# Performance work log

Measured on AMD Instinct MI355X. Metric: run time of the kernel, lower is better.

The kernel has to match this reference:

```python
import jax, jax.numpy as jnp
import numpy as np
from jax import lax

DN = ('NCHW', 'OIHW', 'NCHW')

def _conv(x, w, b, stride):
    y = lax.conv_general_dilated(x, w, (stride, stride), [(1, 1), (1, 1)], dimension_numbers=DN)
    return y + b[None, :, None, None]

def _deconv(x, w, b):
    # ConvTranspose2d(k=4, stride=2, pad=1) == conv with lhs_dilation=2, pad=k-1-p=2,
    # with w already in flipped OIHW layout.
    y = lax.conv_general_dilated(x, w, (1, 1), [(2, 2), (2, 2)], lhs_dilation=(2, 2), dimension_numbers=DN)
    return y + b[None, :, None, None]

def setup_inputs() -> dict:
    key = jax.random.key(0)
    ks = jax.random.split(key, 14)
    s = 0.05  # keep activations numerically tame
    return {
        'x':   jax.random.normal(ks[0], (16, 3, 256, 256), jnp.float32),
        'ew1': jax.random.normal(ks[1], (64, 3, 4, 4), jnp.float32) * s,
        'eb1': jax.random.normal(ks[2], (64,), jnp.float32) * s,
        'ew2': jax.random.normal(ks[3], (128, 64, 4, 4), jnp.float32) * s,
        'eb2': jax.random.normal(ks[4], (128,), jnp.float32) * s,
        'ew3': jax.random.normal(ks[5], (256, 128, 4, 4), jnp.float32) * s,
        'eb3': jax.random.normal(ks[6], (256,), jnp.float32) * s,
        'cb':  jax.random.normal(ks[7], (8192, 256), jnp.float32),
        'dw1': jax.random.normal(ks[8], (128, 256, 4, 4), jnp.float32) * s,
        'db1': jax.random.normal(ks[9], (128,), jnp.float32) * s,
        'dw2': jax.random.normal(ks[10], (64, 128, 4, 4), jnp.float32) * s,
        'db2': jax.random.normal(ks[11], (64,), jnp.float32) * s,
        'dw3': jax.random.normal(ks[12], (3, 64, 4, 4), jnp.float32) * s,
        'db3': jax.random.normal(ks[13], (3,), jnp.float32) * s,
    }

def reference(x, ew1, eb1, ew2, eb2, ew3, eb3, cb, dw1, db1, dw2, db2, dw3, db3):
    # encoder: 3 stride-2 convs with ReLU between
    h = jax.nn.relu(_conv(x, ew1, eb1, 2))
    h = jax.nn.relu(_conv(h, ew2, eb2, 2))
    feat = _conv(h, ew3, eb3, 2)                     # [B, 256, 32, 32]
    B, C, H, W = feat.shape
    flat = feat.reshape(B, C, H * W).transpose(0, 2, 1)  # [B, HW, C]
    scores = jnp.einsum('btc,kc->btk', flat, cb)     # [B, HW, K] large matrix
    indices = jnp.argmax(scores, axis=-1)            # [B, HW]
    quantized = cb[indices]                          # [B, HW, C]
    q = quantized.transpose(0, 2, 1).reshape(B, C, H, W)
    # decoder: 3 stride-2 transposed convs with ReLU between
    d = jax.nn.relu(_deconv(q, dw1, db1))
    d = jax.nn.relu(_deconv(d, dw2, db2))
    recon = _deconv(d, dw3, db3)                     # [B, 3, 256, 256]
    return recon, indices
```

## Files before the change

kernel.cpp:

```cpp
#include <hip/hip_runtime.h>
#include <hip/hip_fp16.h>
#include <cstdint>
#include <cstddef>

typedef __attribute__((ext_vector_type(8))) short short8;
typedef __attribute__((ext_vector_type(8))) _Float16 h16x8;
typedef __attribute__((ext_vector_type(4))) float f32x4;

__device__ __forceinline__ short f2bf(float x) {
  union { float f; unsigned u; } a; a.f = x;
  unsigned r = a.u + 0x7fff + ((a.u >> 16) & 1);
  return (short)(r >> 16);
}
__device__ __forceinline__ float bf2f(short s) {
  union { unsigned u; float f; } a;
  a.u = ((unsigned)(unsigned short)s) << 16; return a.f;
}
__device__ __forceinline__ void fsplit16(float v, short& h, short& l) {
  __half a = __float2half(v);
  h = (short)__half_as_ushort(a);
  l = (short)__half_as_ushort(__float2half(v - __half2float(a)));
}

__device__ __forceinline__ void ld16(const void* g, void* l) {
  __builtin_amdgcn_global_load_lds(
      (const __attribute__((address_space(1))) unsigned int*)g,
      (__attribute__((address_space(3))) unsigned int*)l, 16, 0, 0);
}

__global__ __launch_bounds__(256) void conv1_kernel(
    const float* __restrict__ x, const float* __restrict__ w,
    const float* __restrict__ bias, short* __restrict__ yh, short* __restrict__ yl)
{
  __shared__ __align__(16) float wl[64 * 48];
  __shared__ float bl[64];
  const int tid = threadIdx.x;
  for (int i = tid; i < 64 * 48; i += 256) wl[i] = w[i];
  if (tid < 64) bl[tid] = bias[tid];
  __syncthreads();
  const int n  = blockIdx.y;
  const int oh = blockIdx.x * 2 + (tid >> 7);
  const int ow = tid & 127;
  const float* xb = x + (size_t)n * 3 * 65536;
  const int ih0 = oh * 2 - 1, iw0 = ow * 2 - 1;
  float xin[48];
#pragma unroll
  for (int ic = 0; ic < 3; ++ic)
#pragma unroll
    for (int kh = 0; kh < 4; ++kh) {
      int ih = ih0 + kh;
      bool rok = (unsigned)ih < 256u;
#pragma unroll
      for (int kw = 0; kw < 4; ++kw) {
        int iw = iw0 + kw;
        xin[ic * 16 + kh * 4 + kw] =
            (rok && (unsigned)iw < 256u) ? xb[ic * 65536 + ih * 256 + iw] : 0.f;
      }
    }
  const size_t ob = ((size_t)n * 16384 + oh * 128 + ow) * 64;
  for (int g = 0; g < 8; ++g) {
    short hs[8], ls[8];
#pragma unroll
    for (int j = 0; j < 8; ++j) {
      const int oc = g * 8 + j;
      float acc = bl[oc];
      const float* wo = &wl[oc * 48];
#pragma unroll
      for (int t = 0; t < 48; ++t) acc = fmaf(wo[t], xin[t], acc);
      acc = fmaxf(acc, 0.f) * 64.f;
      fsplit16(acc, hs[j], ls[j]);
    }
    *(short8*)(yh + ob + g * 8) = *(short8*)hs;
    *(short8*)(yl + ob + g * 8) = *(short8*)ls;
  }
}

template <int COUT, int CIN>
__global__ __launch_bounds__(256) void wpack_conv(
    const float* __restrict__ w, short* __restrict__ Wh, short* __restrict__ Wl)
{
  constexpr int K = 16 * CIN;
  const int idx = blockIdx.x * 256 + threadIdx.x;
  const int oc = idx / K, k = idx - oc * K;
  const int kk = k / CIN, ic = k - kk * CIN;
  const int kh = kk >> 2, kw = kk & 3;
  float v = w[(((size_t)oc * CIN + ic) * 4 + kh) * 4 + kw] * 64.f;
  short h, l;
  fsplit16(v, h, l);
  Wh[idx] = h;
  Wl[idx] = l;
}

template <int CIN, int HIN, int COUTT, bool RELU, bool OUTF>
__global__ __launch_bounds__(256) void conv_mfma(
    const short* __restrict__ inh, const short* __restrict__ inl,
    const short* __restrict__ Wph, const short* __restrict__ Wpl,
    const float* __restrict__ bias,
    short* __restrict__ outh, short* __restrict__ outl,
    float* __restrict__ outf)
{
  constexpr int K = 16 * CIN;
  constexpr int HOUT = HIN / 2;
  constexpr int MT = 128, NPX = 128;
  constexpr int GS = (HOUT == 64) ? 6 : 5;
  constexpr int AE = 4 * MT;
  constexpr int NS = K / 32;
  constexpr float RS = 1.f / 4096.f;
  __shared__ __align__(16) short AhL[2][AE * 8];
  __shared__ __align__(16) short AlL[2][AE * 8];
  __shared__ __align__(16) float bl[MT];
  const int tid = threadIdx.x;
  const int w = tid >> 6, lane = tid & 63;
  const int wm = w >> 1, wn = w & 1;
  const int kgl = lane >> 4, cl = lane & 15;
  const int n = blockIdx.z;
  const int oc0 = blockIdx.y * MT;
  const int oh0 = blockIdx.x * (NPX / HOUT);
  if (tid < MT) bl[tid] = bias[oc0 + tid];

  f32x4 acc[4][4];
#pragma unroll
  for (int i = 0; i < 4; ++i)
#pragma unroll
    for (int j = 0; j < 4; ++j) acc[i][j] = (f32x4){0.f, 0.f, 0.f, 0.f};

  auto stageA = [&](int s, int b) {
    const int kc = s * 32;
#pragma unroll
    for (int rep = 0; rep < AE / 256; ++rep) {
      int e = rep * 256 + tid;
      int kg = e >> 7, oc_l = e & (MT - 1);
      size_t go = (size_t)(oc0 + oc_l) * K + kc + kg * 8;
      int lo = (e & ~63) * 8;
      ld16(Wph + go, &AhL[b][lo]);
      ld16(Wpl + go, &AlL[b][lo]);
    }
  };
  const h16x8 zzh = {0, 0, 0, 0, 0, 0, 0, 0};
  auto loadB = [&](int s, h16x8* bh, h16x8* blv) {
    const int kc = s * 32;
    const int kk = kc / CIN, ic0 = kc % CIN;
    const int kh = kk >> 2, kw = kk & 3;
#pragma unroll
    for (int nt = 0; nt < 4; ++nt) {
      int m = wn * 64 + nt * 16 + cl;
      int ih = 2 * (oh0 + (m >> GS)) - 1 + kh;
      int iw = 2 * (m & (HOUT - 1)) - 1 + kw;
      bool ok = ((unsigned)ih < (unsigned)HIN) && ((unsigned)iw < (unsigned)HIN);
      size_t go = ok ? ((size_t)((n * HIN + ih) * HIN + iw) * CIN + ic0 + kgl * 8)
                     : (size_t)(ic0 + kgl * 8);
      h16x8 vh = *(const h16x8*)(inh + go);
      h16x8 vl = *(const h16x8*)(inl + go);
      bh[nt] = ok ? vh : zzh;
      blv[nt] = ok ? vl : zzh;
    }
  };
  auto compute = [&](int b, const h16x8* bh, const h16x8* blv) {
    h16x8 ah[4], al[4];
#pragma unroll
    for (int mt = 0; mt < 4; ++mt) {
      int row = kgl * MT + wm * 64 + mt * 16 + cl;
      ah[mt] = *(const h16x8*)&AhL[b][row * 8];
      al[mt] = *(const h16x8*)&AlL[b][row * 8];
    }
#pragma unroll
    for (int mt = 0; mt < 4; ++mt)
#pragma unroll
      for (int nt = 0; nt < 4; ++nt) {
        acc[mt][nt] = __builtin_amdgcn_mfma_f32_16x16x32_f16(
            ah[mt], bh[nt], acc[mt][nt], 0, 0, 0);
        acc[mt][nt] = __builtin_amdgcn_mfma_f32_16x16x32_f16(
            ah[mt], blv[nt], acc[mt][nt], 0, 0, 0);
        acc[mt][nt] = __builtin_amdgcn_mfma_f32_16x16x32_f16(
            al[mt], bh[nt], acc[mt][nt], 0, 0, 0);
      }
  };

  h16x8 bhA[4], blA[4], bhB[4], blB[4];
  stageA(0, 0);
  loadB(0, bhA, blA);
  __syncthreads();
  for (int s2 = 0; s2 < NS; s2 += 2) {
    stageA(s2 + 1, 1);
    loadB(s2 + 1, bhB, blB);
    compute(0, bhA, blA);
    __syncthreads();
    if (s2 + 2 < NS) { stageA(s2 + 2, 0); loadB(s2 + 2, bhA, blA); }
    compute(1, bhB, blB);
    __syncthreads();
  }
#pragma unroll
  for (int mt = 0; mt < 4; ++mt) {
    const int oc = wm * 64 + mt * 16 + kgl * 4;
    const float4 bv = *(const float4*)&bl[oc];
#pragma unroll
    for (int nt = 0; nt < 4; ++nt) {
      const int px = wn * 64 + nt * 16 + cl;
      const int oh = oh0 + (px >> GS), ow = px & (HOUT - 1);
      const size_t ob =
          ((size_t)n * (HOUT * HOUT) + oh * HOUT + ow) * COUTT + oc0 + oc;
      float v0 = acc[mt][nt][0] * RS + bv.x;
      float v1 = acc[mt][nt][1] * RS + bv.y;
      float v2 = acc[mt][nt][2] * RS + bv.z;
      float v3 = acc[mt][nt][3] * RS + bv.w;
      if (RELU) {
        v0 = fmaxf(v0, 0.f); v1 = fmaxf(v1, 0.f);
        v2 = fmaxf(v2, 0.f); v3 = fmaxf(v3, 0.f);
      }
      if constexpr (OUTF) {
        ushort4 s;
        s.x = __half_as_ushort(__float2half(v0));
        s.y = __half_as_ushort(__float2half(v1));
        s.z = __half_as_ushort(__float2half(v2));
        s.w = __half_as_ushort(__float2half(v3));
        *(ushort4*)((unsigned short*)outh + ob) = s;
        *(float4*)(outf + ob) = make_float4(v0, v1, v2, v3);
      } else {
        short4 hh, ll;
        fsplit16(v0 * 64.f, hh.x, ll.x);
        fsplit16(v1 * 64.f, hh.y, ll.y);
        fsplit16(v2 * 64.f, hh.z, ll.z);
        fsplit16(v3 * 64.f, hh.w, ll.w);
        *(short4*)(outh + ob) = hh;
        *(short4*)(outl + ob) = ll;
      }
    }
  }
}

__global__ __launch_bounds__(256) void cb_convert(
    const float* __restrict__ cb, short* __restrict__ cbh,
    short* __restrict__ cbl, short* __restrict__ cb16)
{
  const int g = blockIdx.x * 256 + threadIdx.x;
  const float* p = cb + (size_t)g * 8;
  short hs[8], ls[8], fs[8];
#pragma unroll
  for (int u = 0; u < 8; ++u) {
    float v = p[u];
    short h = f2bf(v);
    hs[u] = h;
    ls[u] = f2bf(v - bf2f(h));
    fs[u] = (short)__half_as_ushort(__float2half(v));
  }
  *(short8*)(cbh + (size_t)g * 8) = *(short8*)hs;
  *(short8*)(cbl + (size_t)g * 8) = *(short8*)ls;
  *(short8*)(cb16 + (size_t)g * 8) = *(short8*)fs;
}

__global__ __launch_bounds__(256, 2) void vq_mfma(
    const short* __restrict__ cb16, const short* __restrict__ ft16,
    float4* __restrict__ t4v)
{
  __shared__ __align__(16) short Ah[3][4 * 128 * 8];
  __shared__ __align__(16) float MrgV[256 * 4];
  const int tid = threadIdx.x;
  const int w = tid >> 6, lane = tid & 63;
  const int wm = w >> 1, wn = w & 1;
  const int tok0 = blockIdx.x * 128;
  const int split = blockIdx.y;
  const int kgl = lane >> 4, cl = lane & 15;
  const int i0 = w * 128;

  h16x8 breg[8][4];
#pragma unroll
  for (int s = 0; s < 8; ++s)
#pragma unroll
    for (int nt = 0; nt < 4; ++nt)
      breg[s][nt] = *(const h16x8*)(ft16 +
          ((size_t)(tok0 + wn * 64 + nt * 16 + cl)) * 256 + s * 32 + kgl * 8);

  auto stageA = [&](int g, int b) {
    const int tile = g >> 3, s = g & 7;
    const int code0 = split * 1024 + tile * 128;
    const int kc = s * 32;
#pragma unroll
    for (int rep = 0; rep < 2; ++rep) {
      int ib = i0 + rep * 64;
      int i = ib + lane;
      int m = i & 127, kg = i >> 7;
      size_t go = (size_t)(code0 + m) * 256 + kc + kg * 8;
      ld16(cb16 + go, &Ah[b][ib * 8]);
    }
  };

  f32x4 acc[4][4];

  float m1[4], m2[4];
#pragma unroll
  for (int nt = 0; nt < 4; ++nt) { m1[nt] = -3.4e38f; m2[nt] = -3.4e38f; }
  const unsigned orbase0 = (unsigned)(wm * 64 + kgl * 4);
  auto fold = [&](int tile) {
    const unsigned orb = (unsigned)(tile * 128) + orbase0;
#pragma unroll
    for (int nt = 0; nt < 4; ++nt)
#pragma unroll
      for (int mt = 0; mt < 4; ++mt)
#pragma unroll
        for (int r = 0; r < 4; ++r) {
          union { float f; unsigned u; } pv;
          pv.f = acc[mt][nt][r];
          pv.u = (pv.u & 0xFFFFF800u) | (orb + (unsigned)(mt * 16 + r));
          float t = fminf(m1[nt], pv.f);
          m1[nt] = fmaxf(m1[nt], pv.f);
          m2[nt] = fmaxf(m2[nt], t);
        }
  };

  auto computeS = [&](int b, int s_static, bool first) {
    h16x8 ah[4];
#pragma unroll
    for (int mt = 0; mt < 4; ++mt) {
      int row = wm * 64 + mt * 16 + cl;
      ah[mt] = *(const h16x8*)&Ah[b][(kgl * 128 + row) * 8];
    }
    if (first) {
      f32x4 z4 = (f32x4){0.f, 0.f, 0.f, 0.f};
#pragma unroll
      for (int mt = 0; mt < 4; ++mt)
#pragma unroll
        for (int nt = 0; nt < 4; ++nt)
          acc[mt][nt] = __builtin_amdgcn_mfma_f32_16x16x32_f16(
              ah[mt], breg[s_static][nt], z4, 0, 0, 0);
    } else {
#pragma unroll
      for (int mt = 0; mt < 4; ++mt)
#pragma unroll
        for (int nt = 0; nt < 4; ++nt)
          acc[mt][nt] = __builtin_amdgcn_mfma_f32_16x16x32_f16(
              ah[mt], breg[s_static][nt], acc[mt][nt], 0, 0, 0);
    }
  };

  stageA(0, 0);
  stageA(1, 1);
  asm volatile("s_waitcnt vmcnt(0)" ::: "memory");
  __builtin_amdgcn_sched_barrier(0);
  __builtin_amdgcn_s_barrier();
  for (int tile = 0; tile < 7; ++tile) {
#pragma unroll
    for (int s = 0; s < 8; ++s) {
      const int g = tile * 8 + s;
      asm volatile("s_waitcnt vmcnt(2)" ::: "memory");
      __builtin_amdgcn_sched_barrier(0);
      __builtin_amdgcn_s_barrier();
      computeS(g % 3, s, s == 0);
      stageA(g + 2, (g + 2) % 3);
    }
    fold(tile);
  }
#pragma unroll
  for (int s = 0; s < 8; ++s) {
    const int g = 56 + s;
    if (s < 7) {
      asm volatile("s_waitcnt vmcnt(2)" ::: "memory");
    } else {
      asm volatile("s_waitcnt vmcnt(0)" ::: "memory");
    }
    __builtin_amdgcn_sched_barrier(0);
    __builtin_amdgcn_s_barrier();
    computeS(g % 3, s, s == 0);
    if (g + 2 < 64) stageA(g + 2, (g + 2) % 3);
  }
  fold(7);

#pragma unroll
  for (int nt = 0; nt < 4; ++nt) {
    float mv[4] = {m1[nt], m2[nt], -3.4e38f, -3.4e38f};
#pragma unroll
    for (int st = 16; st < 64; st <<= 1) {
      float ov[4];
#pragma unroll
      for (int k = 0; k < 4; ++k) ov[k] = __shfl_xor(mv[k], st);
#pragma unroll
      for (int k = 0; k < 4; ++k) {
        if (ov[k] > mv[3]) {
          mv[3] = ov[k];
#pragma unroll
          for (int q = 3; q > 0; --q)
            if (mv[q] > mv[q - 1]) {
              float tv = mv[q]; mv[q] = mv[q - 1]; mv[q - 1] = tv;
            }
        }
      }
    }
    if (lane < 16) {
      int tl = wn * 64 + nt * 16 + cl;
#pragma unroll
      for (int k = 0; k < 4; ++k) MrgV[(wm * 128 + tl) * 4 + k] = mv[k];
    }
  }
  __syncthreads();
  if (tid < 128) {
    int tl = tid;
    float mv[4];
#pragma unroll
    for (int k = 0; k < 4; ++k) mv[k] = MrgV[tl * 4 + k];
#pragma unroll
    for (int k = 0; k < 4; ++k) {
      float ov = MrgV[(128 + tl) * 4 + k];
      if (ov > mv[3]) {
        mv[3] = ov;
#pragma unroll
        for (int q = 3; q > 0; --q)
          if (mv[q] > mv[q - 1]) {
            float tv = mv[q]; mv[q] = mv[q - 1]; mv[q - 1] = tv;
          }
      }
    }
    size_t o = (size_t)split * 16384 + tok0 + tl;
    t4v[o] = make_float4(mv[0], mv[1], mv[2], mv[3]);
  }
}

__global__ __launch_bounds__(256) void vq_rescore(
    const float4* __restrict__ t4v, const float* __restrict__ featc,
    const float* __restrict__ cb, int* __restrict__ fidx,
    float* __restrict__ idx_out)
{
  const int t = blockIdx.x * 256 + threadIdx.x;
  float vs[4] = {-3.4e38f, -3.4e38f, -3.4e38f, -3.4e38f};
  int is[4] = {0, 0, 0, 0};
#pragma unroll
  for (int sp = 0; sp < 8; ++sp) {
    float4 v4 = t4v[(size_t)sp * 16384 + t];
    float vv[4] = {v4.x, v4.y, v4.z, v4.w};
#pragma unroll
    for (int k = 0; k < 4; ++k) {
      float v = vv[k];
      union { float f; unsigned u; } pu; pu.f = v;
      int ii = sp * 1024 + (int)(pu.u & 0x7FFu);
      if (v > vs[3]) {
        vs[3] = v; is[3] = ii;
#pragma unroll
        for (int q = 3; q > 0; --q)
          if (vs[q] > vs[q - 1]) {
            float tv = vs[q]; vs[q] = vs[q - 1]; vs[q - 1] = tv;
            int ti = is[q]; is[q] = is[q - 1]; is[q - 1] = ti;
          }
      }
    }
  }
  const float4* fc = (const float4*)(featc + (size_t)t * 256);
  const float4* c0 = (const float4*)(cb + (size_t)is[0] * 256);
  const float4* c1 = (const float4*)(cb + (size_t)is[1] * 256);
  const float4* c2 = (const float4*)(cb + (size_t)is[2] * 256);
  const float4* c3 = (const float4*)(cb + (size_t)is[3] * 256);
  float s0 = 0.f, s1 = 0.f, s2 = 0.f, s3 = 0.f;
  for (int k4 = 0; k4 < 64; ++k4) {
    float4 f = fc[k4];
    float4 w0 = c0[k4], w1 = c1[k4], w2 = c2[k4], w3 = c3[k4];
    s0 = fmaf(w0.x, f.x, fmaf(w0.y, f.y, fmaf(w0.z, f.z, fmaf(w0.w, f.w, s0))));
    s1 = fmaf(w1.x, f.x, fmaf(w1.y, f.y, fmaf(w1.z, f.z, fmaf(w1.w, f.w, s1))));
    s2 = fmaf(w2.x, f.x, fmaf(w2.y, f.y, fmaf(w2.z, f.z, fmaf(w2.w, f.w, s2))));
    s3 = fmaf(w3.x, f.x, fmaf(w3.y, f.y, fmaf(w3.z, f.z, fmaf(w3.w, f.w, s3))));
  }
  float best = s0; int bi = is[0];
  float sv[3] = {s1, s2, s3};
  int si2[3] = {is[1], is[2], is[3]};
#pragma unroll
  for (int c = 0; c < 3; ++c)
    if (sv[c] > best || (sv[c] == best && si2[c] < bi)) { best = sv[c]; bi = si2[c]; }
  fidx[t] = bi;
  idx_out[t] = (float)bi;
}

template <int COUT, int CIN>
__global__ __launch_bounds__(256) void wpack(
    const float* __restrict__ w, short* __restrict__ Ah, short* __restrict__ Al)
{
  constexpr int K = 4 * CIN;
  const int idx = blockIdx.x * 256 + threadIdx.x;
  const int par = idx / (COUT * K);
  const int rem = idx % (COUT * K);
  const int oc = rem / K;
  const int k = rem % K;
  const int kk = k / CIN, ic = k % CIN;
  const int kh = 2 * (kk >> 1) + (par >> 1);
  const int kw = 2 * (kk & 1) + (par & 1);
  float v = w[(((size_t)oc * CIN + ic) * 4 + kh) * 4 + kw];
  short h = f2bf(v);
  Ah[idx] = h;
  Al[idx] = f2bf(v - bf2f(h));
}

__global__ __launch_bounds__(256) void gather2(
    const short* __restrict__ cbh, const short* __restrict__ cbl,
    const int* __restrict__ fidx, short* __restrict__ qTh, short* __restrict__ qTl)
{
  const int tid = threadIdx.x;
  const int gt = blockIdx.x * 64 + (tid >> 2);
  const int part = tid & 3;
  const int code = fidx[gt];
  const short8* sh = (const short8*)(cbh + (size_t)code * 256 + part * 64);
  const short8* sl = (const short8*)(cbl + (size_t)code * 256 + part * 64);
  short8* dh = (short8*)(qTh + (size_t)gt * 256 + part * 64);
  short8* dl = (short8*)(qTl + (size_t)gt * 256 + part * 64);
#pragma unroll
  for (int j = 0; j < 8; ++j) { dh[j] = sh[j]; dl[j] = sl[j]; }
}

template <int CIN, int GRID, int COUT, int NPX, int WM, int WN, bool OUT_HALF>
__global__ __launch_bounds__(256) void deconv_mfma(
    const short* __restrict__ inh, const short* __restrict__ inl,
    const short* __restrict__ Aph, const short* __restrict__ Apl,
    const float* __restrict__ bias, void* __restrict__ out_h,
    void* __restrict__ out_l)
{
  constexpr int K = 4 * CIN, HOUT = 2 * GRID, AE = 4 * COUT;
  constexpr int GS = (GRID == 32) ? 5 : 6;
  constexpr int NS = K / 32;
  __shared__ __align__(16) short AhL[2][AE * 8];
  __shared__ __align__(16) short AlL[2][AE * 8];
  __shared__ float bl[COUT];
  const int tid = threadIdx.x;
  const int w = tid >> 6, lane = tid & 63;
  const int wm = w / WN, wn = w % WN;
  const int kgl = lane >> 4, cl = lane & 15;
  const int par = blockIdx.y, n = blockIdx.z;
  const int pr = par >> 1, pc = par & 1;
  const int Ut0 = blockIdx.x * (NPX / GRID);
  if (tid < COUT) bl[tid] = bias[tid];

  f32x4 acc[4][4];
#pragma unroll
  for (int i = 0; i < 4; ++i)
#pragma unroll
    for (int j = 0; j < 4; ++j) acc[i][j] = (f32x4){0.f, 0.f, 0.f, 0.f};

  auto stageA = [&](int s, int b) {
    const int kc = s * 32;
#pragma unroll
    for (int rep = 0; rep < AE / 256; ++rep) {
      int e = rep * 256 + tid;
      int kg = e / COUT, oc_l = e % COUT;
      size_t go = ((size_t)(par * COUT + oc_l)) * K + kc + kg * 8;
      int lo = (e & ~63) * 8;
      ld16(Aph + go, &AhL[b][lo]);
      ld16(Apl + go, &AlL[b][lo]);
    }
  };
  const short8 zz = {0, 0, 0, 0, 0, 0, 0, 0};
  auto loadB = [&](int s, short8* bh, short8* blo) {
    const int kc = s * 32;
    const int kk = kc / CIN, ic0 = kc % CIN;
    const int dr = (kk >> 1) + pr - 1, dc = (kk & 1) + pc - 1;
#pragma unroll
    for (int nt = 0; nt < 4; ++nt) {
      int m = wn * 64 + nt * 16 + cl;
      int sU = Ut0 + (m >> GS) + dr;
      int sV = (m & (GRID - 1)) + dc;
      bool ok = (unsigned)sU < (unsigned)GRID && (unsigned)sV < (unsigned)GRID;
      long pix = (long)(n * GRID + sU) * GRID + sV;
      size_t go = ok ? (size_t)(pix * CIN + ic0 + kgl * 8)
                     : (size_t)(ic0 + kgl * 8);
      short8 vh = *(const short8*)(inh + go);
      short8 vl = *(const short8*)(inl + go);
      bh[nt] = ok ? vh : zz;
      blo[nt] = ok ? vl : zz;
    }
  };
  auto compute = [&](int b, const short8* bh, const short8* blo) {
    short8 ah[4], al[4];
#pragma unroll
    for (int mt = 0; mt < 4; ++mt) {
      int row = kgl * COUT + wm * 64 + mt * 16 + cl;
      ah[mt] = *(const short8*)&AhL[b][row * 8];
      al[mt] = *(const short8*)&AlL[b][row * 8];
    }
#pragma unroll
    for (int mt = 0; mt < 4; ++mt)
#pragma unroll
      for (int nt = 0; nt < 4; ++nt) {
        acc[mt][nt] = __builtin_amdgcn_mfma_f32_16x16x32_bf16(
            ah[mt], bh[nt], acc[mt][nt], 0, 0, 0);
        acc[mt][nt] = __builtin_amdgcn_mfma_f32_16x16x32_bf16(
            ah[mt], blo[nt], acc[mt][nt], 0, 0, 0);
        acc[mt][nt] = __builtin_amdgcn_mfma_f32_16x16x32_bf16(
            al[mt], bh[nt], acc[mt][nt], 0, 0, 0);
      }
  };

  short8 bhA[4], blA[4], bhB[4], blB[4];
  stageA(0, 0);
  loadB(0, bhA, blA);
  __syncthreads();
  for (int s2 = 0; s2 < NS; s2 += 2) {
    stageA(s2 + 1, 1);
    loadB(s2 + 1, bhB, blB);
    compute(0, bhA, blA);
    __syncthreads();
    if (s2 + 2 < NS) { stageA(s2 + 2, 0); loadB(s2 + 2, bhA, blA); }
    compute(1, bhB, blB);
    __syncthreads();
  }
#pragma unroll
  for (int mt = 0; mt < 4; ++mt) {
    const int oc = wm * 64 + mt * 16 + kgl * 4;
    const float4 bv = *(const float4*)&bl[oc];
#pragma unroll
    for (int nt = 0; nt < 4; ++nt) {
      const int px = wn * 64 + nt * 16 + cl;
      const int U = Ut0 + (px >> GS), V = px & (GRID - 1);
      const int r = 2 * U + pr, c = 2 * V + pc;
      const size_t ob = ((size_t)n * HOUT * HOUT + (size_t)r * HOUT + c) * COUT + oc;
      float v0 = fmaxf(acc[mt][nt][0] + bv.x, 0.f);
      float v1 = fmaxf(acc[mt][nt][1] + bv.y, 0.f);
      float v2 = fmaxf(acc[mt][nt][2] + bv.z, 0.f);
      float v3 = fmaxf(acc[mt][nt][3] + bv.w, 0.f);
      if constexpr (OUT_HALF) {
        ushort4 s;
        s.x = __half_as_ushort(__float2half(v0));
        s.y = __half_as_ushort(__float2half(v1));
        s.z = __half_as_ushort(__float2half(v2));
        s.w = __half_as_ushort(__float2half(v3));
        *(ushort4*)((unsigned short*)out_h + ob) = s;
      } else {
        short4 hh, ll;
        hh.x = f2bf(v0); ll.x = f2bf(v0 - bf2f(hh.x));
        hh.y = f2bf(v1); ll.y = f2bf(v1 - bf2f(hh.y));
        hh.z = f2bf(v2); ll.z = f2bf(v2 - bf2f(hh.z));
        hh.w = f2bf(v3); ll.w = f2bf(v3 - bf2f(hh.w));
        *(short4*)((short*)out_h + ob) = hh;
        *(short4*)((short*)out_l + ob) = ll;
      }
    }
  }
}

__global__ __launch_bounds__(256) void deconv3_kernel(
    const __half* __restrict__ d2, const float* __restrict__ w,
    const float* __restrict__ bias, float* __restrict__ y)
{
  __shared__ __align__(16) float Xl[108 * 68];
  __shared__ __align__(16) float wl[4 * 4 * 3 * 64];
  const int tid = threadIdx.x;
  for (int i = tid; i < 3072; i += 256) {
    int oc = i >> 10, ic = (i >> 4) & 63, kh = (i >> 2) & 3, kw = i & 3;
    int par = (kh & 1) * 2 + (kw & 1), kidx = (kh >> 1) * 2 + (kw >> 1);
    wl[((par * 4 + kidx) * 3 + oc) * 64 + ic] = w[i];
  }
  const int n = blockIdx.z, r0 = blockIdx.y * 8, c0 = blockIdx.x * 32;
  const int gr0 = (r0 >> 1) - 1, gc0 = (c0 >> 1) - 1;
  for (int e = tid; e < 1728; e += 256) {
    int pl = e >> 4, sub = e & 15;
    int rr = pl / 18, cc = pl - rr * 18;
    int gr = gr0 + rr, gc = gc0 + cc;
    float4 v = make_float4(0.f, 0.f, 0.f, 0.f);
    if ((unsigned)gr < 128u && (unsigned)gc < 128u) {
      const __half2* p =
          (const __half2*)(d2 + ((size_t)(n * 16384 + gr * 128 + gc) * 64 + sub * 4));
      float2 f0 = __half22float2(p[0]);
      float2 f1 = __half22float2(p[1]);
      v = make_float4(f0.x, f0.y, f1.x, f1.y);
    }
    *(float4*)&Xl[pl * 68 + sub * 4] = v;
  }
  __syncthreads();
  const int wv = tid >> 6, lane = tid & 63;
  const int pr = wv >> 1, pc = wv & 1;
  const int Ul = lane >> 4, Vl = lane & 15;
  float a0 = bias[0], a1 = bias[1], a2 = bias[2];
  const int parb = wv * 768;
#pragma unroll
  for (int ic4 = 0; ic4 < 16; ++ic4) {
    float4 xv[4];
#pragma unroll
    for (int t = 0; t < 4; ++t) {
      int lr = Ul + (t >> 1) + pr, lc = Vl + (t & 1) + pc;
      xv[t] = *(const float4*)&Xl[(lr * 18 + lc) * 68 + ic4 * 4];
    }
#pragma unroll
    for (int t = 0; t < 4; ++t) {
      float4 w0 = *(const float4*)&wl[parb + (t * 3 + 0) * 64 + ic4 * 4];
      float4 w1 = *(const float4*)&wl[parb + (t * 3 + 1) * 64 + ic4 * 4];
      float4 w2 = *(const float4*)&wl[parb + (t * 3 + 2) * 64 + ic4 * 4];
      a0 = fmaf(w0.x, xv[t].x, fmaf(w0.y, xv[t].y, fmaf(w0.z, xv[t].z, fmaf(w0.w, xv[t].w, a0))));
      a1 = fmaf(w1.x, xv[t].x, fmaf(w1.y, xv[t].y, fmaf(w1.z, xv[t].z, fmaf(w1.w, xv[t].w, a1))));
      a2 = fmaf(w2.x, xv[t].x, fmaf(w2.y, xv[t].y, fmaf(w2.z, xv[t].z, fmaf(w2.w, xv[t].w, a2))));
    }
  }
  const int r = r0 + 2 * Ul + pr, c = c0 + 2 * Vl + pc;
  float* yn = y + (size_t)n * 3 * 65536 + r * 256 + c;
  yn[0] = a0;
  yn[65536] = a1;
  yn[131072] = a2;
}

extern "C" void kernel_launch(void* const* d_in, const int* in_sizes, int n_in,
                              void* d_out, int out_size, void* d_ws, size_t ws_size,
                              hipStream_t stream)
{
  const float* x   = (const float*)d_in[0];
  const float* ew1 = (const float*)d_in[1];
  const float* eb1 = (const float*)d_in[2];
  const float* ew2 = (const float*)d_in[3];
  const float* eb2 = (const float*)d_in[4];
  const float* ew3 = (const float*)d_in[5];
  const float* eb3 = (const float*)d_in[6];
  const float* cb  = (const float*)d_in[7];
  const float* dw1 = (const float*)d_in[8];
  const float* db1 = (const float*)d_in[9];
  const float* dw2 = (const float*)d_in[10];
  const float* db2 = (const float*)d_in[11];
  const float* dw3 = (const float*)d_in[12];
  const float* db3 = (const float*)d_in[13];

  float* recon = (float*)d_out;
  float* idxf  = (float*)d_out + 3145728;

  const size_t MB = 1048576ull;
  char* ws = (char*)d_ws;
  short* h1h = (short*)ws;
  short* h1l = (short*)(ws + 32 * MB);
  short* h2h = (short*)(ws + 64 * MB);
  short* h2l = (short*)(ws + 80 * MB);
  short* ft16  = (short*)ws;
  float* featf = (float*)(ws + 16 * MB);
  short* cbh  = (short*)(ws + 64 * MB);
  short* cbl  = (short*)(ws + 68 * MB);
  short* cb16 = (short*)(ws + 72 * MB);
  float4* t4v = (float4*)(ws + 80 * MB);
  int*    fidx = (int*)(ws + 92 * MB);
  short* A1h = (short*)(ws + 76 * MB);
  short* A1l = (short*)(ws + 77 * MB);
  short* A2h = (short*)(ws + 78 * MB);
  short* A2l = (short*)(ws + 78 * MB + 262144);
  short* qTh = (short*)ws;
  short* qTl = (short*)(ws + 8 * MB);
  short* d1h = (short*)(ws + 32 * MB);
  short* d1l = (short*)(ws + 48 * MB);
  __half* d2 = (__half*)ws;
  short* W2h = (short*)recon;
  short* W2l = W2h + 131072;
  short* W3h = W2h + 262144;
  short* W3l = W2h + 786432;

  conv1_kernel<<<dim3(64, 16), 256, 0, stream>>>(x, ew1, eb1, h1h, h1l);
  wpack_conv<128, 64><<<dim3(512), 256, 0, stream>>>(ew2, W2h, W2l);
  conv_mfma<64, 128, 128, true, false><<<dim3(32, 1, 16), 256, 0, stream>>>(
      h1h, h1l, W2h, W2l, eb2, h2h, h2l, nullptr);
  wpack_conv<256, 128><<<dim3(2048), 256, 0, stream>>>(ew3, W3h, W3l);
  conv_mfma<128, 64, 256, false, true><<<dim3(8, 2, 16), 256, 0, stream>>>(
      h2h, h2l, W3h, W3l, eb3, ft16, nullptr, featf);

  cb_convert<<<dim3(1024), 256, 0, stream>>>(cb, cbh, cbl, cb16);
  vq_mfma<<<dim3(128, 8), 256, 0, stream>>>(cb16, ft16, t4v);
  vq_rescore<<<dim3(64), 256, 0, stream>>>(t4v, featf, cb, fidx, idxf);

  wpack<128, 256><<<dim3(2048), 256, 0, stream>>>(dw1, A1h, A1l);
  wpack<64, 128><<<dim3(512), 256, 0, stream>>>(dw2, A2h, A2l);
  gather2<<<dim3(256), 256, 0, stream>>>(cbh, cbl, fidx, qTh, qTl);

  deconv_mfma<256, 32, 128, 128, 2, 2, false>
      <<<dim3(8, 4, 16), 256, 0, stream>>>(qTh, qTl, A1h, A1l, db1, d1h, d1l);
  deconv_mfma<128, 64, 64, 256, 1, 4, true>
      <<<dim3(16, 4, 16), 256, 0, stream>>>(d1h, d1l, A2h, A2l, db2, d2, d2);
  deconv3_kernel<<<dim3(8, 32, 16), 256, 0, stream>>>(d2, dw3, db3, recon);
}
```

Before: 828.0 us.

## Triple-buffer LDS stages with explicit vmcnt waits and single barrier per step

The conv and deconv MFMA kernels move from double-buffered LDS staging with two __syncthreads per pair of k-steps to a triple-buffered ring. Each step now uses an explicit s_waitcnt vmcnt on the outstanding async global-to-LDS loads plus one s_barrier. Loads for step s+2 are issued right after computing step s, so two stages stay in flight and the memory latency is better hidden. In exchange, LDS use per block grows by half, which may lower occupancy. The hand-coded vmcnt counts must match the exact number of loads each stage issues, or the kernels can read stale data.

```diff
diff --git a/kernel.cpp b/kernel.cpp
--- a/kernel.cpp
+++ b/kernel.cpp
@@ -106,8 +106,8 @@
   constexpr int AE = 4 * MT;
   constexpr int NS = K / 32;
   constexpr float RS = 1.f / 4096.f;
-  __shared__ __align__(16) short AhL[2][AE * 8];
-  __shared__ __align__(16) short AlL[2][AE * 8];
+  __shared__ __align__(16) short AhL[3][AE * 8];
+  __shared__ __align__(16) short AlL[3][AE * 8];
   __shared__ __align__(16) float bl[MT];
   const int tid = threadIdx.x;
   const int w = tid >> 6, lane = tid & 63;
@@ -179,15 +179,23 @@
   h16x8 bhA[4], blA[4], bhB[4], blB[4];
   stageA(0, 0);
   loadB(0, bhA, blA);
-  __syncthreads();
+  stageA(1, 1);
+  loadB(1, bhB, blB);
   for (int s2 = 0; s2 < NS; s2 += 2) {
-    stageA(s2 + 1, 1);
-    loadB(s2 + 1, bhB, blB);
-    compute(0, bhA, blA);
-    __syncthreads();
-    if (s2 + 2 < NS) { stageA(s2 + 2, 0); loadB(s2 + 2, bhA, blA); }
-    compute(1, bhB, blB);
-    __syncthreads();
+    asm volatile("s_waitcnt vmcnt(12)" ::: "memory");
+    __builtin_amdgcn_sched_barrier(0);
+    __builtin_amdgcn_s_barrier();
+    compute(s2 % 3, bhA, blA);
+    if (s2 + 2 < NS) { stageA(s2 + 2, (s2 + 2) % 3); loadB(s2 + 2, bhA, blA); }
+    if (s2 + 2 < NS) {
+      asm volatile("s_waitcnt vmcnt(12)" ::: "memory");
+    } else {
+      asm volatile("s_waitcnt vmcnt(0)" ::: "memory");
+    }
+    __builtin_amdgcn_sched_barrier(0);
+    __builtin_amdgcn_s_barrier();
+    compute((s2 + 1) % 3, bhB, blB);
+    if (s2 + 3 < NS) { stageA(s2 + 3, (s2 + 3) % 3); loadB(s2 + 3, bhB, blB); }
   }
 #pragma unroll
   for (int mt = 0; mt < 4; ++mt) {
@@ -510,8 +518,9 @@
   constexpr int K = 4 * CIN, HOUT = 2 * GRID, AE = 4 * COUT;
   constexpr int GS = (GRID == 32) ? 5 : 6;
   constexpr int NS = K / 32;
-  __shared__ __align__(16) short AhL[2][AE * 8];
-  __shared__ __align__(16) short AlL[2][AE * 8];
+  constexpr int VC = (AE / 256) * 2 + 8;
+  __shared__ __align__(16) short AhL[3][AE * 8];
+  __shared__ __align__(16) short AlL[3][AE * 8];
   __shared__ float bl[COUT];
   const int tid = threadIdx.x;
   const int w = tid >> 6, lane = tid & 63;
@@ -584,15 +593,31 @@
   short8 bhA[4], blA[4], bhB[4], blB[4];
   stageA(0, 0);
   loadB(0, bhA, blA);
-  __syncthreads();
+  stageA(1, 1);
+  loadB(1, bhB, blB);
   for (int s2 = 0; s2 < NS; s2 += 2) {
-    stageA(s2 + 1, 1);
-    loadB(s2 + 1, bhB, blB);
-    compute(0, bhA, blA);
-    __syncthreads();
-    if (s2 + 2 < NS) { stageA(s2 + 2, 0); loadB(s2 + 2, bhA, blA); }
-    compute(1, bhB, blB);
-    __syncthreads();
+    if constexpr (VC == 12) {
+      asm volatile("s_waitcnt vmcnt(12)" ::: "memory");
+    } else {
+      asm volatile("s_waitcnt vmcnt(10)" ::: "memory");
+    }
+    __builtin_amdgcn_sched_barrier(0);
+    __builtin_amdgcn_s_barrier();
+    compute(s2 % 3, bhA, blA);
+    if (s2 + 2 < NS) { stageA(s2 + 2, (s2 + 2) % 3); loadB(s2 + 2, bhA, blA); }
+    if (s2 + 2 < NS) {
+      if constexpr (VC == 12) {
+        asm volatile("s_waitcnt vmcnt(12)" ::: "memory");
+      } else {
+        asm volatile("s_waitcnt vmcnt(10)" ::: "memory");
+      }
+    } else {
+      asm volatile("s_waitcnt vmcnt(0)" ::: "memory");
+    }
+    __builtin_amdgcn_sched_barrier(0);
+    __builtin_amdgcn_s_barrier();
+    compute((s2 + 1) % 3, bhB, blB);
+    if (s2 + 3 < NS) { stageA(s2 + 3, (s2 + 3) % 3); loadB(s2 + 3, bhB, blB); }
   }
 #pragma unroll
   for (int mt = 0; mt < 4; ++mt) {
```

New measurement: 860.8 us. +4.0%, slower.

## Load conv/deconv weight fragments directly from global, dropping LDS staging and barriers

Applied to the files above, without the earlier changes.

Both the encoder conv and decoder deconv MFMA kernels stop staging weight tiles into double-buffered shared memory. Each lane now reads its A fragments straight from global memory through precomputed row pointers inside a simple K loop unrolled by two. Bias is also read from global in the epilogue. This removes the LDS traffic and __syncthreads barriers and frees LDS for occupancy. In exchange, warps sharing the same weights issue redundant global loads, and the explicit software prefetch of the next stage is gone, so latency hiding now depends on the compiler and on occupancy.

```diff
diff --git a/kernel.cpp b/kernel.cpp
--- a/kernel.cpp
+++ b/kernel.cpp
@@ -103,12 +103,8 @@
   constexpr int HOUT = HIN / 2;
   constexpr int MT = 128, NPX = 128;
   constexpr int GS = (HOUT == 64) ? 6 : 5;
-  constexpr int AE = 4 * MT;
   constexpr int NS = K / 32;
   constexpr float RS = 1.f / 4096.f;
-  __shared__ __align__(16) short AhL[2][AE * 8];
-  __shared__ __align__(16) short AlL[2][AE * 8];
-  __shared__ __align__(16) float bl[MT];
   const int tid = threadIdx.x;
   const int w = tid >> 6, lane = tid & 63;
   const int wm = w >> 1, wn = w & 1;
@@ -116,7 +112,6 @@
   const int n = blockIdx.z;
   const int oc0 = blockIdx.y * MT;
   const int oh0 = blockIdx.x * (NPX / HOUT);
-  if (tid < MT) bl[tid] = bias[oc0 + tid];
 
   f32x4 acc[4][4];
 #pragma unroll
@@ -124,26 +119,33 @@
 #pragma unroll
     for (int j = 0; j < 4; ++j) acc[i][j] = (f32x4){0.f, 0.f, 0.f, 0.f};
 
-  auto stageA = [&](int s, int b) {
-    const int kc = s * 32;
-#pragma unroll
-    for (int rep = 0; rep < AE / 256; ++rep) {
-      int e = rep * 256 + tid;
-      int kg = e >> 7, oc_l = e & (MT - 1);
-      size_t go = (size_t)(oc0 + oc_l) * K + kc + kg * 8;
-      int lo = (e & ~63) * 8;
-      ld16(Wph + go, &AhL[b][lo]);
-      ld16(Wpl + go, &AlL[b][lo]);
-    }
-  };
+  const short* pWh[4];
+  const short* pWl[4];
+#pragma unroll
+  for (int mt = 0; mt < 4; ++mt) {
+    size_t ro = (size_t)(oc0 + wm * 64 + mt * 16 + cl) * K + kgl * 8;
+    pWh[mt] = Wph + ro;
+    pWl[mt] = Wpl + ro;
+  }
   const h16x8 zzh = {0, 0, 0, 0, 0, 0, 0, 0};
-  auto loadB = [&](int s, h16x8* bh, h16x8* blv) {
+  int bm[4];
+#pragma unroll
+  for (int nt = 0; nt < 4; ++nt) bm[nt] = wn * 64 + nt * 16 + cl;
+
+#pragma unroll 2
+  for (int s = 0; s < NS; ++s) {
     const int kc = s * 32;
     const int kk = kc / CIN, ic0 = kc % CIN;
     const int kh = kk >> 2, kw = kk & 3;
+    h16x8 ah[4], al[4], bh[4], blv[4];
+#pragma unroll
+    for (int mt = 0; mt < 4; ++mt) {
+      ah[mt] = *(const h16x8*)(pWh[mt] + kc);
+      al[mt] = *(const h16x8*)(pWl[mt] + kc);
+    }
 #pragma unroll
     for (int nt = 0; nt < 4; ++nt) {
-      int m = wn * 64 + nt * 16 + cl;
+      int m = bm[nt];
       int ih = 2 * (oh0 + (m >> GS)) - 1 + kh;
       int iw = 2 * (m & (HOUT - 1)) - 1 + kw;
       bool ok = ((unsigned)ih < (unsigned)HIN) && ((unsigned)iw < (unsigned)HIN);
@@ -154,15 +156,6 @@
       bh[nt] = ok ? vh : zzh;
       blv[nt] = ok ? vl : zzh;
     }
-  };
-  auto compute = [&](int b, const h16x8* bh, const h16x8* blv) {
-    h16x8 ah[4], al[4];
-#pragma unroll
-    for (int mt = 0; mt < 4; ++mt) {
-      int row = kgl * MT + wm * 64 + mt * 16 + cl;
-      ah[mt] = *(const h16x8*)&AhL[b][row * 8];
-      al[mt] = *(const h16x8*)&AlL[b][row * 8];
-    }
 #pragma unroll
     for (int mt = 0; mt < 4; ++mt)
 #pragma unroll
@@ -174,25 +167,11 @@
         acc[mt][nt] = __builtin_amdgcn_mfma_f32_16x16x32_f16(
             al[mt], bh[nt], acc[mt][nt], 0, 0, 0);
       }
-  };
-
-  h16x8 bhA[4], blA[4], bhB[4], blB[4];
-  stageA(0, 0);
-  loadB(0, bhA, blA);
-  __syncthreads();
-  for (int s2 = 0; s2 < NS; s2 += 2) {
-    stageA(s2 + 1, 1);
-    loadB(s2 + 1, bhB, blB);
-    compute(0, bhA, blA);
-    __syncthreads();
-    if (s2 + 2 < NS) { stageA(s2 + 2, 0); loadB(s2 + 2, bhA, blA); }
-    compute(1, bhB, blB);
-    __syncthreads();
   }
 #pragma unroll
   for (int mt = 0; mt < 4; ++mt) {
     const int oc = wm * 64 + mt * 16 + kgl * 4;
-    const float4 bv = *(const float4*)&bl[oc];
+    const float4 bv = *(const float4*)&bias[oc0 + oc];
 #pragma unroll
     for (int nt = 0; nt < 4; ++nt) {
       const int px = wn * 64 + nt * 16 + cl;
@@ -507,12 +486,9 @@
     const float* __restrict__ bias, void* __restrict__ out_h,
     void* __restrict__ out_l)
 {
-  constexpr int K = 4 * CIN, HOUT = 2 * GRID, AE = 4 * COUT;
+  constexpr int K = 4 * CIN, HOUT = 2 * GRID;
   constexpr int GS = (GRID == 32) ? 5 : 6;
   constexpr int NS = K / 32;
-  __shared__ __align__(16) short AhL[2][AE * 8];
-  __shared__ __align__(16) short AlL[2][AE * 8];
-  __shared__ float bl[COUT];
   const int tid = threadIdx.x;
   const int w = tid >> 6, lane = tid & 63;
   const int wm = w / WN, wn = w % WN;
@@ -520,7 +496,6 @@
   const int par = blockIdx.y, n = blockIdx.z;
   const int pr = par >> 1, pc = par & 1;
   const int Ut0 = blockIdx.x * (NPX / GRID);
-  if (tid < COUT) bl[tid] = bias[tid];
 
   f32x4 acc[4][4];
 #pragma unroll
@@ -528,26 +503,33 @@
 #pragma unroll
     for (int j = 0; j < 4; ++j) acc[i][j] = (f32x4){0.f, 0.f, 0.f, 0.f};
 
-  auto stageA = [&](int s, int b) {
-    const int kc = s * 32;
-#pragma unroll
-    for (int rep = 0; rep < AE / 256; ++rep) {
-      int e = rep * 256 + tid;
-      int kg = e / COUT, oc_l = e % COUT;
-      size_t go = ((size_t)(par * COUT + oc_l)) * K + kc + kg * 8;
-      int lo = (e & ~63) * 8;
-      ld16(Aph + go, &AhL[b][lo]);
-      ld16(Apl + go, &AlL[b][lo]);
-    }
-  };
+  const short* pAh[4];
+  const short* pAl[4];
+#pragma unroll
+  for (int mt = 0; mt < 4; ++mt) {
+    size_t ro = ((size_t)(par * COUT + wm * 64 + mt * 16 + cl)) * K + kgl * 8;
+    pAh[mt] = Aph + ro;
+    pAl[mt] = Apl + ro;
+  }
   const short8 zz = {0, 0, 0, 0, 0, 0, 0, 0};
-  auto loadB = [&](int s, short8* bh, short8* blo) {
+  int bm[4];
+#pragma unroll
+  for (int nt = 0; nt < 4; ++nt) bm[nt] = wn * 64 + nt * 16 + cl;
+
+#pragma unroll 2
+  for (int s = 0; s < NS; ++s) {
     const int kc = s * 32;
     const int kk = kc / CIN, ic0 = kc % CIN;
     const int dr = (kk >> 1) + pr - 1, dc = (kk & 1) + pc - 1;
+    short8 ah[4], al[4], bh[4], blo[4];
+#pragma unroll
+    for (int mt = 0; mt < 4; ++mt) {
+      ah[mt] = *(const short8*)(pAh[mt] + kc);
+      al[mt] = *(const short8*)(pAl[mt] + kc);
+    }
 #pragma unroll
     for (int nt = 0; nt < 4; ++nt) {
-      int m = wn * 64 + nt * 16 + cl;
+      int m = bm[nt];
       int sU = Ut0 + (m >> GS) + dr;
       int sV = (m & (GRID - 1)) + dc;
       bool ok = (unsigned)sU < (unsigned)GRID && (unsigned)sV < (unsigned)GRID;
@@ -559,15 +541,6 @@
       bh[nt] = ok ? vh : zz;
       blo[nt] = ok ? vl : zz;
     }
-  };
-  auto compute = [&](int b, const short8* bh, const short8* blo) {
-    short8 ah[4], al[4];
-#pragma unroll
-    for (int mt = 0; mt < 4; ++mt) {
-      int row = kgl * COUT + wm * 64 + mt * 16 + cl;
-      ah[mt] = *(const short8*)&AhL[b][row * 8];
-      al[mt] = *(const short8*)&AlL[b][row * 8];
-    }
 #pragma unroll
     for (int mt = 0; mt < 4; ++mt)
 #pragma unroll
@@ -579,25 +552,11 @@
         acc[mt][nt] = __builtin_amdgcn_mfma_f32_16x16x32_bf16(
             al[mt], bh[nt], acc[mt][nt], 0, 0, 0);
       }
-  };
-
-  short8 bhA[4], blA[4], bhB[4], blB[4];
-  stageA(0, 0);
-  loadB(0, bhA, blA);
-  __syncthreads();
-  for (int s2 = 0; s2 < NS; s2 += 2) {
-    stageA(s2 + 1, 1);
-    loadB(s2 + 1, bhB, blB);
-    compute(0, bhA, blA);
-    __syncthreads();
-    if (s2 + 2 < NS) { stageA(s2 + 2, 0); loadB(s2 + 2, bhA, blA); }
-    compute(1, bhB, blB);
-    __syncthreads();
   }
 #pragma unroll
   for (int mt = 0; mt < 4; ++mt) {
     const int oc = wm * 64 + mt * 16 + kgl * 4;
-    const float4 bv = *(const float4*)&bl[oc];
+    const float4 bv = *(const float4*)&bias[oc];
 #pragma unroll
     for (int nt = 0; nt < 4; ++nt) {
       const int px = wn * 64 + nt * 16 + cl;
```

Result: slower. 889.8 us (+7.5%).
